# Kernel optimization log

Measured on AMD Instinct MI355X. Metric: run time of the kernel, lower is better.

Reference implementation:

```python
import jax, jax.numpy as jnp
import numpy as np

D_MODEL = 1024
NHEAD = 8
HEAD_DIM = D_MODEL // NHEAD
D_FF = 4096
EPS_ATTN = 1e-6
EPS_LN = 1e-5


def _layernorm(x, g, b):
    mu = jnp.mean(x, axis=-1, keepdims=True)
    var = jnp.var(x, axis=-1, keepdims=True)
    return (x - mu) * jax.lax.rsqrt(var + EPS_LN) * g + b


def _linear_attention(q, k, v):
    # q,k,v: [N, L, H, D]
    Q = jax.nn.elu(q) + 1.0
    K = jax.nn.elu(k) + 1.0
    v_length = v.shape[1]
    v = v / v_length
    KV = jnp.einsum('nshd,nshv->nhdv', K, v)           # [N,H,D,D]
    Z = 1.0 / (jnp.einsum('nlhd,nhd->nlh', Q, K.sum(axis=1)) + EPS_ATTN)
    out = jnp.einsum('nlhd,nhdv,nlh->nlhv', Q, KV, Z) * v_length
    return out


def setup_inputs() -> dict:
    key = jax.random.key(0)
    ks = jax.random.split(key, 12)
    s = 1.0 / np.sqrt(D_MODEL)
    sf = 1.0 / np.sqrt(D_FF)
    return {
        'x': jax.random.normal(ks[0], (2, 4096, D_MODEL), jnp.float32),
        'wq': jax.random.normal(ks[1], (D_MODEL, D_MODEL), jnp.float32) * s,
        'wk': jax.random.normal(ks[2], (D_MODEL, D_MODEL), jnp.float32) * s,
        'wv': jax.random.normal(ks[3], (D_MODEL, D_MODEL), jnp.float32) * s,
        'w1': jax.random.normal(ks[4], (D_FF, D_MODEL), jnp.float32) * s,
        'b1': jnp.zeros((D_FF,), jnp.float32),
        'w2': jax.random.normal(ks[5], (D_MODEL, D_FF), jnp.float32) * sf,
        'b2': jnp.zeros((D_MODEL,), jnp.float32),
        'g1': jnp.ones((D_MODEL,), jnp.float32),
        'be1': jnp.zeros((D_MODEL,), jnp.float32),
        'g2': jnp.ones((D_MODEL,), jnp.float32),
        'be2': jnp.zeros((D_MODEL,), jnp.float32),
    }


def reference(x, wq, wk, wv, w1, b1, w2, b2, g1, be1, g2, be2):
    N, L, C = x.shape
    # pre-norm self attention
    x2 = _layernorm(x, g1, be1)
    q = (x2 @ wq.T).reshape(N, L, NHEAD, HEAD_DIM)
    k = (x2 @ wk.T).reshape(N, L, NHEAD, HEAD_DIM)
    v = (x2 @ wv.T).reshape(N, L, NHEAD, HEAD_DIM)
    msg = _linear_attention(q, k, v).reshape(N, L, C)
    x = x + msg
    # MLP block
    x2 = _layernorm(x, g2, be2)
    h = jax.nn.gelu(x2 @ w1.T + b1, approximate=False)
    x = x + (h @ w2.T + b2)
    return x
```

## Files before the change

kernel.cpp:

```cpp
#include <hip/hip_runtime.h>
#include <hip/hip_bf16.h>
#include <math.h>

typedef __bf16 bf16x8 __attribute__((ext_vector_type(8)));
typedef float f32x4 __attribute__((ext_vector_type(4)));

#define DEVI __device__ __forceinline__

DEVI void gload_lds16(const __bf16* g, __bf16* l) {
    __builtin_amdgcn_global_load_lds(
        (const __attribute__((address_space(1))) void*)g,
        (__attribute__((address_space(3))) void*)l, 16, 0, 0);
}

__global__ void sniff_kernel(const unsigned short* __restrict__ x, int* flags) {
    const int tid = threadIdx.x;
    const unsigned short u = x[tid * 2];
    const int e = (u >> 7) & 0xFF;
    const int zero = (u == 0) ? 1 : 0;
    const int sane = ((e >= 0x71 && e <= 0x8E) || ((u & 0x7FFF) == 0)) ? 1 : 0;
    const unsigned long long mz = __ballot(zero != 0);
    const unsigned long long ms = __ballot(sane != 0);
    __shared__ int wz[4], wsn[4];
    if ((tid & 63) == 0) { wz[tid >> 6] = __popcll(mz); wsn[tid >> 6] = __popcll(ms); }
    __syncthreads();
    if (tid == 0) {
        const int nz = wz[0] + wz[1] + wz[2] + wz[3];
        const int ns = wsn[0] + wsn[1] + wsn[2] + wsn[3];
        flags[0] = (nz >= 192 || ns < 128) ? 1 : 0;
    }
}

__global__ __launch_bounds__(256) void convert_kernel(const void* __restrict__ src,
                                                      __bf16* __restrict__ dst, int n,
                                                      const int* __restrict__ flags) {
    const int i = (blockIdx.x * 256 + threadIdx.x) * 8;
    if (i >= n) return;
    if (flags[0]) {
        const float* s = (const float*)src;
        bf16x8 o;
#pragma unroll
        for (int j = 0; j < 8; j++) o[j] = (__bf16)s[i + j];
        *(bf16x8*)(dst + i) = o;
    } else {
        *(uint4*)(dst + i) = *(const uint4*)((const __bf16*)src + i);
    }
}

template <typename T>
__global__ __launch_bounds__(256) void ln_kernel(const T* __restrict__ x,
                                                 const __bf16* __restrict__ g,
                                                 const __bf16* __restrict__ b,
                                                 __bf16* __restrict__ out) {
    const size_t row = blockIdx.x;
    const T* xr = x + row * 1024;
    const int tid = threadIdx.x;
    float v[4];
#pragma unroll
    for (int i = 0; i < 4; i++) v[i] = (float)xr[tid * 4 + i];
    float s = v[0] + v[1] + v[2] + v[3];
    float s2 = v[0] * v[0] + v[1] * v[1] + v[2] * v[2] + v[3] * v[3];
#pragma unroll
    for (int m = 32; m >= 1; m >>= 1) {
        s += __shfl_xor(s, m, 64);
        s2 += __shfl_xor(s2, m, 64);
    }
    __shared__ float rs[4], rs2[4];
    const int wave = tid >> 6, lane = tid & 63;
    if (lane == 0) { rs[wave] = s; rs2[wave] = s2; }
    __syncthreads();
    s = rs[0] + rs[1] + rs[2] + rs[3];
    s2 = rs2[0] + rs2[1] + rs2[2] + rs2[3];
    const float mu = s * (1.0f / 1024.0f);
    const float var = s2 * (1.0f / 1024.0f) - mu * mu;
    const float inv = rsqrtf(var + 1e-5f);
#pragma unroll
    for (int i = 0; i < 4; i++) {
        const int c = tid * 4 + i;
        out[row * 1024 + c] = (__bf16)((v[i] - mu) * inv * (float)g[c] + (float)b[c]);
    }
}

enum { EP_NONE = 0, EP_ELU1 = 1, EP_BIAS_GELU = 2, EP_BIAS_RES = 3, EP_QKV = 4 };

#define READMM(RA, RB)                                                        \
    do {                                                                      \
        bf16x8 af_[4], bfv_[4];                                               \
        _Pragma("unroll") for (int i_ = 0; i_ < 4; i_++) {                    \
            af_[i_]  = *(const bf16x8*)&RA[(wm * 64 + i_ * 16 + lm) * 32 + swz]; \
            bfv_[i_] = *(const bf16x8*)&RB[(wn * 64 + i_ * 16 + lm) * 32 + swz]; \
        }                                                                     \
        _Pragma("unroll") for (int i_ = 0; i_ < 4; i_++)                      \
            _Pragma("unroll") for (int j_ = 0; j_ < 4; j_++)                  \
                acc[i_][j_] = __builtin_amdgcn_mfma_f32_16x16x32_bf16(        \
                    af_[i_], bfv_[j_], acc[i_][j_], 0, 0, 0);                 \
    } while (0)

#define KBODY(RA, RB, SA, SB, TS, WAITN)                                      \
    do {                                                                      \
        asm volatile("s_waitcnt vmcnt(" #WAITN ")" ::: "memory");             \
        __builtin_amdgcn_s_barrier();                                         \
        __builtin_amdgcn_sched_barrier(0);                                    \
        if ((TS) < nt) {                                                      \
            const int k0_ = (TS) << 5;                                        \
            gload_lds16(pa0 + k0_, &SA[tid * 8]);                             \
            gload_lds16(pa1 + k0_, &SA[2048 + tid * 8]);                      \
            gload_lds16(pb0 + k0_, &SB[tid * 8]);                             \
            gload_lds16(pb1 + k0_, &SB[2048 + tid * 8]);                      \
        }                                                                     \
        __builtin_amdgcn_s_setprio(1);                                        \
        READMM(RA, RB);                                                       \
        __builtin_amdgcn_s_setprio(0);                                        \
    } while (0)

template <int EP, typename OutT>
__global__ __launch_bounds__(256, 3) void gemm_bt(
    const __bf16* __restrict__ A, const __bf16* __restrict__ B,
    const __bf16* __restrict__ bias, const float* __restrict__ resid,
    OutT* __restrict__ C, int M, int N, int K) {
    const int gx = gridDim.x, gy = gridDim.y;
    int bm = blockIdx.y, bn = blockIdx.x;
    {
        const int nwg = gx * gy;
        if ((gx & 7) == 0 && (nwg & 63) == 0) {
            const int bid = bm * gx + bn;
            const int perx = nwg >> 3;
            const int gid = (bid & 7) * perx + (bid >> 3);
            const int stg = gid >> 6, pos = gid & 63;
            const int stw = gx >> 3;
            bm = (stg / stw) * 8 + (pos >> 3);
            bn = (stg % stw) * 8 + (pos & 7);
        }
    }
    const int tid = threadIdx.x;
    const int wave = tid >> 6, lane = tid & 63;
    const int wm = wave & 1, wn = wave >> 1;
    const int lm = lane & 15, lq = lane >> 4;
    const int swz = (lq ^ ((lm >> 1) & 3)) * 8;

    __shared__ __align__(16) __bf16 As0[128 * 32];
    __shared__ __align__(16) __bf16 As1[128 * 32];
    __shared__ __align__(16) __bf16 As2[128 * 32];
    __shared__ __align__(16) __bf16 Bs0[128 * 32];
    __shared__ __align__(16) __bf16 Bs1[128 * 32];
    __shared__ __align__(16) __bf16 Bs2[128 * 32];

    f32x4 acc[4][4] = {};

    const int sr = tid >> 2;
    const int sc = (((tid & 3) ^ ((tid >> 3) & 3)) << 3);

    const __bf16* pa0 = A + (size_t)(bm * 128 + sr) * K + sc;
    const __bf16* pa1 = pa0 + (size_t)64 * K;
    const __bf16* pb0 = B + (size_t)(bn * 128 + sr) * K + sc;
    const __bf16* pb1 = pb0 + (size_t)64 * K;

    const int nt = K >> 5;

    gload_lds16(pa0, &As0[tid * 8]);
    gload_lds16(pa1, &As0[2048 + tid * 8]);
    gload_lds16(pb0, &Bs0[tid * 8]);
    gload_lds16(pb1, &Bs0[2048 + tid * 8]);
    if (nt > 1) {
        gload_lds16(pa0 + 32, &As1[tid * 8]);
        gload_lds16(pa1 + 32, &As1[2048 + tid * 8]);
        gload_lds16(pb0 + 32, &Bs1[tid * 8]);
        gload_lds16(pb1 + 32, &Bs1[2048 + tid * 8]);
    }

    int t = 0;
    for (; t + 2 < nt; t += 3) {
        KBODY(As0, Bs0, As2, Bs2, t + 2, 4);
        KBODY(As1, Bs1, As0, Bs0, t + 3, 4);
        KBODY(As2, Bs2, As1, Bs1, t + 4, 4);
    }
    if (t < nt) {
        asm volatile("s_waitcnt vmcnt(0)" ::: "memory");
        __builtin_amdgcn_s_barrier();
        __builtin_amdgcn_sched_barrier(0);
        READMM(As0, Bs0);
        t++;
        if (t < nt) { READMM(As1, Bs1); }
    }

    const int row0 = bm * 128 + wm * 64;
    const int col0 = bn * 128 + wn * 64;
#pragma unroll
    for (int i = 0; i < 4; i++) {
#pragma unroll
        for (int j = 0; j < 4; j++) {
            const int col = col0 + j * 16 + lm;
#pragma unroll
            for (int r = 0; r < 4; r++) {
                const int row = row0 + i * 16 + lq * 4 + r;
                float v = acc[i][j][r];
                if (EP == EP_QKV) {
                    float vv = (col < 2048) ? ((v > 0.0f) ? (v + 1.0f) : expf(v)) : v;
                    __bf16* dst = (col < 1024) ? (__bf16*)C
                                : (col < 2048) ? (__bf16*)const_cast<__bf16*>(bias)
                                               : (__bf16*)const_cast<float*>(resid);
                    dst[(size_t)row * 1024 + (col & 1023)] = (__bf16)vv;
                } else {
                    if (EP == EP_ELU1) {
                        v = (v > 0.0f) ? (v + 1.0f) : expf(v);
                    } else if (EP == EP_BIAS_GELU) {
                        v += (float)bias[col];
                        v = 0.5f * v * (1.0f + erff(v * 0.70710678118654752f));
                    } else if (EP == EP_BIAS_RES) {
                        v += (float)bias[col];
                        v += resid[(size_t)row * N + col];
                    }
                    C[(size_t)row * N + col] = (OutT)v;
                }
            }
        }
    }
}

__global__ __launch_bounds__(256) void kv_kernel(const __bf16* __restrict__ Kf,
                                                 const __bf16* __restrict__ Vf,
                                                 float* __restrict__ pkv,
                                                 float* __restrict__ pks) {
    const int nh = blockIdx.x, sc = blockIdx.y;
    const int n = nh >> 3, h = nh & 7;
    const int tid = threadIdx.x;
    const int tv = tid & 15, td = tid >> 4;
    __shared__ __align__(16) __bf16 Kt[32 * 128];
    __shared__ __align__(16) __bf16 Vt[32 * 128];
    float acc[8][8] = {};
    float ks[8] = {};
    const size_t rowbase = (size_t)n * 4096 + (size_t)sc * 256;
    for (int s0 = 0; s0 < 256; s0 += 32) {
#pragma unroll
        for (int rep = 0; rep < 2; rep++) {
            const int s = tid + rep * 256;
            const int r = s >> 4, cs = (s & 15) * 8;
            const size_t gidx = (rowbase + s0 + r) * 1024 + h * 128 + cs;
            *(bf16x8*)&Kt[r * 128 + cs] = *(const bf16x8*)&Kf[gidx];
            *(bf16x8*)&Vt[r * 128 + cs] = *(const bf16x8*)&Vf[gidx];
        }
        __syncthreads();
#pragma unroll 4
        for (int s = 0; s < 32; s++) {
            const bf16x8 k8 = *(const bf16x8*)&Kt[s * 128 + td * 8];
            const bf16x8 v8 = *(const bf16x8*)&Vt[s * 128 + tv * 8];
            float kk[8], vv[8];
#pragma unroll
            for (int i = 0; i < 8; i++) { kk[i] = (float)k8[i]; vv[i] = (float)v8[i]; }
#pragma unroll
            for (int i = 0; i < 8; i++) {
                ks[i] += kk[i];
#pragma unroll
                for (int j = 0; j < 8; j++) acc[i][j] += kk[i] * vv[j];
            }
        }
        __syncthreads();
    }
    float* dst = pkv + ((size_t)sc * 16 + nh) * 16384;
#pragma unroll
    for (int i = 0; i < 8; i++)
#pragma unroll
        for (int j = 0; j < 8; j++)
            dst[(td * 8 + i) * 128 + tv * 8 + j] = acc[i][j];
    if (tv == 0) {
        float* ds2 = pks + ((size_t)sc * 16 + nh) * 128;
#pragma unroll
        for (int i = 0; i < 8; i++) ds2[td * 8 + i] = ks[i];
    }
}

__global__ __launch_bounds__(256) void kv_reduce(const float* __restrict__ pkv,
                                                 const float* __restrict__ pks,
                                                 __bf16* __restrict__ kvb,
                                                 float* __restrict__ ksf) {
    const int idx = blockIdx.x * 256 + threadIdx.x;
    float s = 0.0f;
#pragma unroll
    for (int c = 0; c < 16; c++) s += pkv[(size_t)c * 262144 + idx];
    kvb[idx] = (__bf16)s;
    if (idx < 2048) {
        float t = 0.0f;
#pragma unroll
        for (int c = 0; c < 16; c++) t += pks[c * 2048 + idx];
        ksf[idx] = t;
    }
}

__global__ __launch_bounds__(256) void z_kernel(const __bf16* __restrict__ Qf,
                                                const float* __restrict__ ksf,
                                                float* __restrict__ zbuf) {
    const int idx = blockIdx.x * 256 + threadIdx.x;
    const int h = idx & 7;
    const size_t row = (size_t)(idx >> 3);
    const __bf16* q = Qf + row * 1024 + h * 128;
    const float* ks = ksf + ((size_t)((row >> 12) * 8 + h)) * 128;
    float s = 0.0f;
    for (int d = 0; d < 128; d += 8) {
        const bf16x8 q8 = *(const bf16x8*)&q[d];
#pragma unroll
        for (int j = 0; j < 8; j++) s += (float)q8[j] * ks[d + j];
    }
    zbuf[idx] = 1.0f / (s + 1e-6f);
}

__global__ __launch_bounds__(256, 2) void attn_out_kernel(
    const __bf16* __restrict__ x, const __bf16* __restrict__ Qf,
    const __bf16* __restrict__ kvb, const float* __restrict__ zbuf,
    float* __restrict__ xmid) {
    const int nh = blockIdx.x, lc = blockIdx.y;
    const int n = nh >> 3, h = nh & 7;
    const int tid = threadIdx.x;
    __shared__ __align__(16) __bf16 KVs[128 * 128];
    __shared__ __align__(16) __bf16 Qs[64 * 128];
    __shared__ float Zs[64];
    const __bf16* kv = kvb + (size_t)nh * 16384;
    for (int i = tid * 8; i < 16384; i += 2048)
        *(bf16x8*)&KVs[i] = *(const bf16x8*)&kv[i];
    const size_t gr0 = (size_t)n * 4096 + (size_t)lc * 64;
#pragma unroll
    for (int rep = 0; rep < 4; rep++) {
        const int s = tid + rep * 256;
        const int r = s >> 4, cs = (s & 15) * 8;
        *(bf16x8*)&Qs[r * 128 + cs] = *(const bf16x8*)&Qf[(gr0 + r) * 1024 + h * 128 + cs];
    }
    if (tid < 64) Zs[tid] = zbuf[(gr0 + tid) * 8 + h];
    __syncthreads();
    const int tv = (tid & 15) * 8;
    const int tr0 = (tid >> 4) * 4;
    float acc[4][8] = {};
    for (int d = 0; d < 128; d++) {
        const bf16x8 kv8 = *(const bf16x8*)&KVs[d * 128 + tv];
        float kf[8];
#pragma unroll
        for (int j = 0; j < 8; j++) kf[j] = (float)kv8[j];
#pragma unroll
        for (int rr = 0; rr < 4; rr++) {
            const float q = (float)Qs[(tr0 + rr) * 128 + d];
#pragma unroll
            for (int j = 0; j < 8; j++) acc[rr][j] += q * kf[j];
        }
    }
#pragma unroll
    for (int rr = 0; rr < 4; rr++) {
        const size_t gi = (gr0 + tr0 + rr) * 1024 + h * 128 + tv;
        const float z = Zs[tr0 + rr];
        const bf16x8 xr = *(const bf16x8*)&x[gi];
#pragma unroll
        for (int j = 0; j < 8; j++) xmid[gi + j] = (float)xr[j] + acc[rr][j] * z;
    }
}

extern "C" void kernel_launch(void* const* d_in, const int* in_sizes, int n_in,
                              void* d_out, int out_size, void* d_ws, size_t ws_size,
                              hipStream_t stream) {
    float* out = (float*)d_out;
    char* ws = (char*)d_ws;

    const int nx = 8388608, nw = 1048576, nw1 = 4194304, nb1 = 4096, ng = 1024;
    size_t off = 0;
    __bf16* cx   = (__bf16*)(ws + off); off += (size_t)nx * 2;
    __bf16* cwq  = (__bf16*)(ws + off); off += (size_t)nw * 2;
    __bf16* cwk  = (__bf16*)(ws + off); off += (size_t)nw * 2;
    __bf16* cwv  = (__bf16*)(ws + off); off += (size_t)nw * 2;
    __bf16* cw1  = (__bf16*)(ws + off); off += (size_t)nw1 * 2;
    __bf16* cb1  = (__bf16*)(ws + off); off += (size_t)nb1 * 2;
    __bf16* cw2  = (__bf16*)(ws + off); off += (size_t)nw1 * 2;
    __bf16* cb2  = (__bf16*)(ws + off); off += (size_t)ng * 2;
    __bf16* cg1  = (__bf16*)(ws + off); off += (size_t)ng * 2;
    __bf16* cbe1 = (__bf16*)(ws + off); off += (size_t)ng * 2;
    __bf16* cg2  = (__bf16*)(ws + off); off += (size_t)ng * 2;
    __bf16* cbe2 = (__bf16*)(ws + off); off += (size_t)ng * 2;
    int* flags = (int*)(ws + off); off += 64;

    char* PB = ws + off;
    __bf16* x2   = (__bf16*)(PB);
    __bf16* Qf   = (__bf16*)(PB + 16777216);
    float*  pkv  = (float*)(PB + 33554432);
    __bf16* hbuf = (__bf16*)(PB + 16777216);
    __bf16* Kf   = (__bf16*)(PB + 50331648);
    __bf16* Vf   = (__bf16*)(PB + 67108864);
    float*  xmid = (float*)(PB + 50331648);
    float*  pks  = (float*)(PB + 83886080);
    float*  ksf  = (float*)(PB + 84017152);
    float*  zbuf = (float*)(PB + 84025344);
    __bf16* kvb  = (__bf16*)(PB + 84287488);

    sniff_kernel<<<1, 256, 0, stream>>>((const unsigned short*)d_in[0], flags);
    convert_kernel<<<nx / 2048, 256, 0, stream>>>(d_in[0], cx, nx, flags);
    convert_kernel<<<nw / 2048, 256, 0, stream>>>(d_in[1], cwq, nw, flags);
    convert_kernel<<<nw / 2048, 256, 0, stream>>>(d_in[2], cwk, nw, flags);
    convert_kernel<<<nw / 2048, 256, 0, stream>>>(d_in[3], cwv, nw, flags);
    convert_kernel<<<nw1 / 2048, 256, 0, stream>>>(d_in[4], cw1, nw1, flags);
    convert_kernel<<<2, 256, 0, stream>>>(d_in[5], cb1, nb1, flags);
    convert_kernel<<<nw1 / 2048, 256, 0, stream>>>(d_in[6], cw2, nw1, flags);
    convert_kernel<<<1, 256, 0, stream>>>(d_in[7], cb2, ng, flags);
    convert_kernel<<<1, 256, 0, stream>>>(d_in[8], cg1, ng, flags);
    convert_kernel<<<1, 256, 0, stream>>>(d_in[9], cbe1, ng, flags);
    convert_kernel<<<1, 256, 0, stream>>>(d_in[10], cg2, ng, flags);
    convert_kernel<<<1, 256, 0, stream>>>(d_in[11], cbe2, ng, flags);

    ln_kernel<__bf16><<<8192, 256, 0, stream>>>(cx, cg1, cbe1, x2);
    gemm_bt<EP_QKV, __bf16><<<dim3(3072 / 128, 8192 / 128), 256, 0, stream>>>(
        x2, cwq, (const __bf16*)Kf, (const float*)Vf, Qf, 8192, 3072, 1024);
    kv_kernel<<<dim3(16, 16), 256, 0, stream>>>(Kf, Vf, pkv, pks);
    kv_reduce<<<1024, 256, 0, stream>>>(pkv, pks, kvb, ksf);
    z_kernel<<<256, 256, 0, stream>>>(Qf, ksf, zbuf);
    attn_out_kernel<<<dim3(16, 64), 256, 0, stream>>>(cx, Qf, kvb, zbuf, xmid);
    ln_kernel<float><<<8192, 256, 0, stream>>>(xmid, cg2, cbe2, x2);
    for (int c = 0; c < 2; c++) {
        const size_t ro = (size_t)c * 4096;
        gemm_bt<EP_BIAS_GELU, __bf16><<<dim3(4096 / 128, 4096 / 128), 256, 0, stream>>>(
            x2 + ro * 1024, cw1, cb1, nullptr, hbuf, 4096, 4096, 1024);
        gemm_bt<EP_BIAS_RES, float><<<dim3(1024 / 128, 4096 / 128), 256, 0, stream>>>(
            hbuf, cw2, cb2, xmid + ro * 1024, out + ro * 1024, 4096, 1024, 4096);
    }
}
```

Measured before the change: 455.0 us.

## Add 256x256-tile 8-wave GEMM with split-K LDS pipeline for QKV and FC1

Adds a new GEMM kernel that uses 256x256 output tiles, 512 threads (8 waves, each computing a 128x64 sub-tile), and a double-buffered LDS pipeline that stages each 64-wide K step as two 32-wide halves. Finer-grained barriers interleave the global-to-LDS loads with the MFMA work. The QKV projection and the FC1+GELU GEMM now use this kernel, while FC2 stays on the old 128x128 kernel. The larger tiles are meant to raise arithmetic intensity and cut global/LDS traffic per FLOP. In exchange the kernel needs 128KB of LDS and many more accumulator registers, which lowers occupancy, and the fewer, larger workgroups may leave CUs idle at the tail.

```diff
diff --git a/kernel.cpp b/kernel.cpp
--- a/kernel.cpp
+++ b/kernel.cpp
@@ -83,34 +83,203 @@
 
 enum { EP_NONE = 0, EP_ELU1 = 1, EP_BIAS_GELU = 2, EP_BIAS_RES = 3, EP_QKV = 4 };
 
-#define READMM(RA, RB)                                                        \
-    do {                                                                      \
-        bf16x8 af_[4], bfv_[4];                                               \
-        _Pragma("unroll") for (int i_ = 0; i_ < 4; i_++) {                    \
-            af_[i_]  = *(const bf16x8*)&RA[(wm * 64 + i_ * 16 + lm) * 32 + swz]; \
+#define STG256(DST, P0, P1, KOFF)                         \
+    do {                                                  \
+        gload_lds16((P0) + (KOFF), &DST[tid * 8]);        \
+        gload_lds16((P1) + (KOFF), &DST[4096 + tid * 8]); \
+    } while (0)
+
+#define MFMA4x4(AV, BV, FRB)                                                   \
+    do {                                                                       \
+        _Pragma("unroll") for (int f_ = 0; f_ < 4; f_++)                       \
+            _Pragma("unroll") for (int c_ = 0; c_ < 4; c_++)                   \
+                acc[(FRB) + f_][c_] = __builtin_amdgcn_mfma_f32_16x16x32_bf16( \
+                    AV[f_], BV[c_], acc[(FRB) + f_][c_], 0, 0, 0);             \
+    } while (0)
+
+#define ITER256(RA0, RA1, RB0, RB1, SA0m, SA1m, SB0m, SB1m, TN, DO_STAGE, VM1) \
+    do {                                                                       \
+        bf16x8 a_[4];                                                          \
+                                    \
+        asm volatile("s_waitcnt vmcnt(4)" ::: "memory");                       \
+        __builtin_amdgcn_s_barrier();                                          \
+        __builtin_amdgcn_sched_barrier(0);                                     \
+        _Pragma("unroll") for (int f_ = 0; f_ < 4; f_++)                       \
+            b0[f_] = *(const bf16x8*)&RB0[boff[f_]];                           \
+        _Pragma("unroll") for (int f_ = 0; f_ < 4; f_++)                       \
+            a_[f_] = *(const bf16x8*)&RA0[aoff[f_]];                           \
+        if (DO_STAGE) STG256(SA0m, sA0, sA1, (TN) * 64);                       \
+        asm volatile("s_waitcnt lgkmcnt(0)" ::: "memory");                     \
+        __builtin_amdgcn_sched_barrier(0);                                     \
+        __builtin_amdgcn_s_setprio(1);                                         \
+        MFMA4x4(a_, b0, 0);                                                    \
+        __builtin_amdgcn_s_setprio(0);                                         \
+                                    \
+        asm volatile("s_waitcnt vmcnt(" #VM1 ")" ::: "memory");                \
+        __builtin_amdgcn_s_barrier();                                          \
+        __builtin_amdgcn_sched_barrier(0);                                     \
+        _Pragma("unroll") for (int f_ = 0; f_ < 4; f_++)                       \
+            b1[f_] = *(const bf16x8*)&RB1[boff[f_]];                           \
+        _Pragma("unroll") for (int f_ = 0; f_ < 4; f_++)                       \
+            a_[f_] = *(const bf16x8*)&RA1[aoff[f_]];                           \
+        if (DO_STAGE) STG256(SB0m, sB0, sB1, (TN) * 64);                       \
+        asm volatile("s_waitcnt lgkmcnt(0)" ::: "memory");                     \
+        __builtin_amdgcn_sched_barrier(0);                                     \
+        __builtin_amdgcn_s_setprio(1);                                         \
+        MFMA4x4(a_, b1, 0);                                                    \
+        __builtin_amdgcn_s_setprio(0);                                         \
+                              \
+        __builtin_amdgcn_s_barrier();                                          \
+        __builtin_amdgcn_sched_barrier(0);                                     \
+        _Pragma("unroll") for (int f_ = 0; f_ < 4; f_++)                       \
+            a_[f_] = *(const bf16x8*)&RA0[aoff[4 + f_]];                       \
+        if (DO_STAGE) STG256(SA1m, sA0, sA1, (TN) * 64 + 32);                  \
+        asm volatile("s_waitcnt lgkmcnt(0)" ::: "memory");                     \
+        __builtin_amdgcn_sched_barrier(0);                                     \
+        __builtin_amdgcn_s_setprio(1);                                         \
+        MFMA4x4(a_, b0, 4);                                                    \
+        __builtin_amdgcn_s_setprio(0);                                         \
+                              \
+        __builtin_amdgcn_s_barrier();                                          \
+        __builtin_amdgcn_sched_barrier(0);                                     \
+        _Pragma("unroll") for (int f_ = 0; f_ < 4; f_++)                       \
+            a_[f_] = *(const bf16x8*)&RA1[aoff[4 + f_]];                       \
+        if (DO_STAGE) STG256(SB1m, sB0, sB1, (TN) * 64 + 32);                  \
+        asm volatile("s_waitcnt lgkmcnt(0)" ::: "memory");                     \
+        __builtin_amdgcn_sched_barrier(0);                                     \
+        __builtin_amdgcn_s_setprio(1);                                         \
+        MFMA4x4(a_, b1, 4);                                                    \
+        __builtin_amdgcn_s_setprio(0);                                         \
+    } while (0)
+
+template <int EP>
+__global__ __launch_bounds__(512, 2) void gemm256(
+    const __bf16* __restrict__ A, const __bf16* __restrict__ B,
+    const __bf16* __restrict__ bias, __bf16* __restrict__ out2,
+    __bf16* __restrict__ out3, __bf16* __restrict__ C, int M, int N, int K) {
+    const int gx = gridDim.x, gy = gridDim.y;
+    int bm = blockIdx.y, bn = blockIdx.x;
+    {
+        const int nwg = gx * gy;
+        const int bid = bm * gx + bn;
+        if ((gx & 7) == 0 && (nwg & 63) == 0) {
+            const int perx = nwg >> 3;
+            const int gid = (bid & 7) * perx + (bid >> 3);
+            const int stg = gid >> 6, pos = gid & 63;
+            const int stw = gx >> 3;
+            bm = (stg / stw) * 8 + (pos >> 3);
+            bn = (stg % stw) * 8 + (pos & 7);
+        } else if ((nwg & 7) == 0) {
+            const int perx = nwg >> 3;
+            const int gid = (bid & 7) * perx + (bid >> 3);
+            bm = gid / gx;
+            bn = gid % gx;
+        }
+    }
+    const int tid = threadIdx.x;
+    const int wave = tid >> 6, lane = tid & 63;
+    const int wr = wave >> 2, wc = wave & 3;
+    const int lm = lane & 15, lq = lane >> 4;
+
+    __shared__ __align__(16) __bf16 A0k0[8192];
+    __shared__ __align__(16) __bf16 A0k1[8192];
+    __shared__ __align__(16) __bf16 B0k0[8192];
+    __shared__ __align__(16) __bf16 B0k1[8192];
+    __shared__ __align__(16) __bf16 A1k0[8192];
+    __shared__ __align__(16) __bf16 A1k1[8192];
+    __shared__ __align__(16) __bf16 B1k0[8192];
+    __shared__ __align__(16) __bf16 B1k1[8192];
+
+    f32x4 acc[8][4] = {};
+    bf16x8 b0[4], b1[4];
+
+    int aoff[8], boff[4];
+#pragma unroll
+    for (int fr = 0; fr < 8; fr++) {
+        const int row = wr * 128 + fr * 16 + lm;
+        aoff[fr] = row * 32 + ((lq ^ (lm & 3)) << 3);
+    }
+#pragma unroll
+    for (int fc = 0; fc < 4; fc++) {
+        const int row = wc * 64 + fc * 16 + lm;
+        boff[fc] = row * 32 + ((lq ^ (lm & 3)) << 3);
+    }
+
+    const int srow = tid >> 2;
+    const int sg = (((tid & 3) ^ ((tid >> 2) & 3)) << 3);
+    const __bf16* sA0 = A + (size_t)(bm * 256 + srow) * K + sg;
+    const __bf16* sA1 = sA0 + (size_t)128 * K;
+    const __bf16* sB0 = B + (size_t)(bn * 256 + srow) * K + sg;
+    const __bf16* sB1 = sB0 + (size_t)128 * K;
+
+    const int nt = K >> 6;
+
+    STG256(A0k0, sA0, sA1, 0);
+    STG256(B0k0, sB0, sB1, 0);
+    STG256(A0k1, sA0, sA1, 32);
+    STG256(B0k1, sB0, sB1, 32);
+
+    int t = 0;
+    for (; t + 2 < nt; t += 2) {
+        ITER256(A0k0, A0k1, B0k0, B0k1, A1k0, A1k1, B1k0, B1k1, t + 1, true, 2);
+        ITER256(A1k0, A1k1, B1k0, B1k1, A0k0, A0k1, B0k0, B0k1, t + 2, true, 2);
+    }
+    ITER256(A0k0, A0k1, B0k0, B0k1, A1k0, A1k1, B1k0, B1k1, t + 1, true, 2);
+    ITER256(A1k0, A1k1, B1k0, B1k1, A0k0, A0k1, B0k0, B0k1, 0, false, 0);
+
+    const int rowb = bm * 256 + wr * 128 + lq * 4;
+    const int colb = bn * 256 + wc * 64 + lm;
+#pragma unroll
+    for (int fr = 0; fr < 8; fr++) {
+#pragma unroll
+        for (int fc = 0; fc < 4; fc++) {
+            const int col = colb + fc * 16;
+#pragma unroll
+            for (int r = 0; r < 4; r++) {
+                const int row = rowb + fr * 16 + r;
+                float v = acc[fr][fc][r];
+                if (EP == EP_QKV) {
+                    float vv = (col < 2048) ? ((v > 0.0f) ? (v + 1.0f) : expf(v)) : v;
+                    __bf16* dst = (col < 1024) ? C : (col < 2048) ? out2 : out3;
+                    dst[(size_t)row * 1024 + (col & 1023)] = (__bf16)vv;
+                } else {
+                    v += (float)bias[col];
+                    v = 0.5f * v * (1.0f + erff(v * 0.70710678118654752f));
+                    C[(size_t)row * N + col] = (__bf16)v;
+                }
+            }
+        }
+    }
+}
+
+#define READMM(RA, RB)                                                           \
+    do {                                                                         \
+        bf16x8 af_[4], bfv_[4];                                                  \
+        _Pragma("unroll") for (int i_ = 0; i_ < 4; i_++) {                       \
+            af_[i_] = *(const bf16x8*)&RA[(wm * 64 + i_ * 16 + lm) * 32 + swz];  \
             bfv_[i_] = *(const bf16x8*)&RB[(wn * 64 + i_ * 16 + lm) * 32 + swz]; \
-        }                                                                     \
-        _Pragma("unroll") for (int i_ = 0; i_ < 4; i_++)                      \
-            _Pragma("unroll") for (int j_ = 0; j_ < 4; j_++)                  \
-                acc[i_][j_] = __builtin_amdgcn_mfma_f32_16x16x32_bf16(        \
-                    af_[i_], bfv_[j_], acc[i_][j_], 0, 0, 0);                 \
+        }                                                                        \
+        _Pragma("unroll") for (int i_ = 0; i_ < 4; i_++)                         \
+            _Pragma("unroll") for (int j_ = 0; j_ < 4; j_++)                     \
+                acc[i_][j_] = __builtin_amdgcn_mfma_f32_16x16x32_bf16(           \
+                    af_[i_], bfv_[j_], acc[i_][j_], 0, 0, 0);                    \
     } while (0)
 
-#define KBODY(RA, RB, SA, SB, TS, WAITN)                                      \
-    do {                                                                      \
-        asm volatile("s_waitcnt vmcnt(" #WAITN ")" ::: "memory");             \
-        __builtin_amdgcn_s_barrier();                                         \
-        __builtin_amdgcn_sched_barrier(0);                                    \
-        if ((TS) < nt) {                                                      \
-            const int k0_ = (TS) << 5;                                        \
-            gload_lds16(pa0 + k0_, &SA[tid * 8]);                             \
-            gload_lds16(pa1 + k0_, &SA[2048 + tid * 8]);                      \
-            gload_lds16(pb0 + k0_, &SB[tid * 8]);                             \
-            gload_lds16(pb1 + k0_, &SB[2048 + tid * 8]);                      \
-        }                                                                     \
-        __builtin_amdgcn_s_setprio(1);                                        \
-        READMM(RA, RB);                                                       \
-        __builtin_amdgcn_s_setprio(0);                                        \
+#define KBODY(RA, RB, SA, SB, TS, WAITN)                           \
+    do {                                                           \
+        asm volatile("s_waitcnt vmcnt(" #WAITN ")" ::: "memory");  \
+        __builtin_amdgcn_s_barrier();                              \
+        __builtin_amdgcn_sched_barrier(0);                         \
+        if ((TS) < nt) {                                           \
+            const int k0_ = (TS) << 5;                             \
+            gload_lds16(pa0 + k0_, &SA[tid * 8]);                  \
+            gload_lds16(pa1 + k0_, &SA[2048 + tid * 8]);           \
+            gload_lds16(pb0 + k0_, &SB[tid * 8]);                  \
+            gload_lds16(pb1 + k0_, &SB[2048 + tid * 8]);           \
+        }                                                          \
+        __builtin_amdgcn_s_setprio(1);                             \
+        READMM(RA, RB);                                            \
+        __builtin_amdgcn_s_setprio(0);                             \
     } while (0)
 
 template <int EP, typename OutT>
@@ -194,24 +363,16 @@
             for (int r = 0; r < 4; r++) {
                 const int row = row0 + i * 16 + lq * 4 + r;
                 float v = acc[i][j][r];
-                if (EP == EP_QKV) {
-                    float vv = (col < 2048) ? ((v > 0.0f) ? (v + 1.0f) : expf(v)) : v;
-                    __bf16* dst = (col < 1024) ? (__bf16*)C
-                                : (col < 2048) ? (__bf16*)const_cast<__bf16*>(bias)
-                                               : (__bf16*)const_cast<float*>(resid);
-                    dst[(size_t)row * 1024 + (col & 1023)] = (__bf16)vv;
-                } else {
-                    if (EP == EP_ELU1) {
-                        v = (v > 0.0f) ? (v + 1.0f) : expf(v);
-                    } else if (EP == EP_BIAS_GELU) {
-                        v += (float)bias[col];
-                        v = 0.5f * v * (1.0f + erff(v * 0.70710678118654752f));
-                    } else if (EP == EP_BIAS_RES) {
-                        v += (float)bias[col];
-                        v += resid[(size_t)row * N + col];
-                    }
-                    C[(size_t)row * N + col] = (OutT)v;
+                if (EP == EP_ELU1) {
+                    v = (v > 0.0f) ? (v + 1.0f) : expf(v);
+                } else if (EP == EP_BIAS_GELU) {
+                    v += (float)bias[col];
+                    v = 0.5f * v * (1.0f + erff(v * 0.70710678118654752f));
+                } else if (EP == EP_BIAS_RES) {
+                    v += (float)bias[col];
+                    v += resid[(size_t)row * N + col];
                 }
+                C[(size_t)row * N + col] = (OutT)v;
             }
         }
     }
@@ -400,8 +561,8 @@
     convert_kernel<<<1, 256, 0, stream>>>(d_in[11], cbe2, ng, flags);
 
     ln_kernel<__bf16><<<8192, 256, 0, stream>>>(cx, cg1, cbe1, x2);
-    gemm_bt<EP_QKV, __bf16><<<dim3(3072 / 128, 8192 / 128), 256, 0, stream>>>(
-        x2, cwq, (const __bf16*)Kf, (const float*)Vf, Qf, 8192, 3072, 1024);
+    gemm256<EP_QKV><<<dim3(3072 / 256, 8192 / 256), 512, 0, stream>>>(
+        x2, cwq, nullptr, Kf, Vf, Qf, 8192, 3072, 1024);
     kv_kernel<<<dim3(16, 16), 256, 0, stream>>>(Kf, Vf, pkv, pks);
     kv_reduce<<<1024, 256, 0, stream>>>(pkv, pks, kvb, ksf);
     z_kernel<<<256, 256, 0, stream>>>(Qf, ksf, zbuf);
@@ -409,8 +570,8 @@
     ln_kernel<float><<<8192, 256, 0, stream>>>(xmid, cg2, cbe2, x2);
     for (int c = 0; c < 2; c++) {
         const size_t ro = (size_t)c * 4096;
-        gemm_bt<EP_BIAS_GELU, __bf16><<<dim3(4096 / 128, 4096 / 128), 256, 0, stream>>>(
-            x2 + ro * 1024, cw1, cb1, nullptr, hbuf, 4096, 4096, 1024);
+        gemm256<EP_BIAS_GELU><<<dim3(4096 / 256, 4096 / 256), 512, 0, stream>>>(
+            x2 + ro * 1024, cw1, cb1, nullptr, nullptr, hbuf, 4096, 4096, 1024);
         gemm_bt<EP_BIAS_RES, float><<<dim3(1024 / 128, 4096 / 128), 256, 0, stream>>>(
             hbuf, cw2, cb2, xmid + ro * 1024, out + ro * 1024, 4096, 1024, 4096);
     }
```

New measurement: 465.0 us. 2.2% more time.

## Fuse Z normalizer into attention output and use 64-row tiles for down-projection

Applied to the files above, without the earlier changes.

The separate z_kernel is removed, and the Q·ksum dot product is now computed inside attn_out_kernel from a shared-memory copy of the key sums, avoiding a launch and a round trip through global memory. The gemm kernel gains a BM template parameter. The second MLP GEMM (N=1024, K=4096) uses 64-row tiles, which doubles its block count from 256 to 512 for better CU occupancy on a small grid. The cost is smaller per-block reuse of B tiles and extra FMAs per d-step in the attention loop.

```diff
diff --git a/kernel.cpp b/kernel.cpp
--- a/kernel.cpp
+++ b/kernel.cpp
@@ -83,37 +83,41 @@
 
 enum { EP_NONE = 0, EP_ELU1 = 1, EP_BIAS_GELU = 2, EP_BIAS_RES = 3, EP_QKV = 4 };
 
-#define READMM(RA, RB)                                                        \
-    do {                                                                      \
-        bf16x8 af_[4], bfv_[4];                                               \
-        _Pragma("unroll") for (int i_ = 0; i_ < 4; i_++) {                    \
-            af_[i_]  = *(const bf16x8*)&RA[(wm * 64 + i_ * 16 + lm) * 32 + swz]; \
-            bfv_[i_] = *(const bf16x8*)&RB[(wn * 64 + i_ * 16 + lm) * 32 + swz]; \
-        }                                                                     \
-        _Pragma("unroll") for (int i_ = 0; i_ < 4; i_++)                      \
-            _Pragma("unroll") for (int j_ = 0; j_ < 4; j_++)                  \
-                acc[i_][j_] = __builtin_amdgcn_mfma_f32_16x16x32_bf16(        \
-                    af_[i_], bfv_[j_], acc[i_][j_], 0, 0, 0);                 \
+#define READMM(RA, RB)                                                            \
+    do {                                                                          \
+        bf16x8 af_[BM / 32], bfv_[4];                                             \
+        _Pragma("unroll") for (int i_ = 0; i_ < BM / 32; i_++)                    \
+            af_[i_] = *(const bf16x8*)&RA[(wm * (BM / 2) + i_ * 16 + lm) * 32 + swz]; \
+        _Pragma("unroll") for (int j_ = 0; j_ < 4; j_++)                          \
+            bfv_[j_] = *(const bf16x8*)&RB[(wn * 64 + j_ * 16 + lm) * 32 + swz];  \
+        _Pragma("unroll") for (int i_ = 0; i_ < BM / 32; i_++)                    \
+            _Pragma("unroll") for (int j_ = 0; j_ < 4; j_++)                      \
+                acc[i_][j_] = __builtin_amdgcn_mfma_f32_16x16x32_bf16(            \
+                    af_[i_], bfv_[j_], acc[i_][j_], 0, 0, 0);                     \
     } while (0)
 
-#define KBODY(RA, RB, SA, SB, TS, WAITN)                                      \
-    do {                                                                      \
-        asm volatile("s_waitcnt vmcnt(" #WAITN ")" ::: "memory");             \
-        __builtin_amdgcn_s_barrier();                                         \
-        __builtin_amdgcn_sched_barrier(0);                                    \
-        if ((TS) < nt) {                                                      \
-            const int k0_ = (TS) << 5;                                        \
-            gload_lds16(pa0 + k0_, &SA[tid * 8]);                             \
-            gload_lds16(pa1 + k0_, &SA[2048 + tid * 8]);                      \
-            gload_lds16(pb0 + k0_, &SB[tid * 8]);                             \
-            gload_lds16(pb1 + k0_, &SB[2048 + tid * 8]);                      \
-        }                                                                     \
-        __builtin_amdgcn_s_setprio(1);                                        \
-        READMM(RA, RB);                                                       \
-        __builtin_amdgcn_s_setprio(0);                                        \
+#define KBODY(RA, RB, SA, SB, TS)                                  \
+    do {                                                           \
+        if constexpr (BM == 128)                                   \
+            asm volatile("s_waitcnt vmcnt(4)" ::: "memory");       \
+        else                                                       \
+            asm volatile("s_waitcnt vmcnt(3)" ::: "memory");       \
+        __builtin_amdgcn_s_barrier();                              \
+        __builtin_amdgcn_sched_barrier(0);                         \
+        if ((TS) < nt) {                                           \
+            const int k0_ = (TS) << 5;                             \
+            gload_lds16(pa0 + k0_, &SA[tid * 8]);                  \
+            if constexpr (BM == 128)                               \
+                gload_lds16(pa1 + k0_, &SA[2048 + tid * 8]);       \
+            gload_lds16(pb0 + k0_, &SB[tid * 8]);                  \
+            gload_lds16(pb1 + k0_, &SB[2048 + tid * 8]);           \
+        }                                                          \
+        __builtin_amdgcn_s_setprio(1);                             \
+        READMM(RA, RB);                                            \
+        __builtin_amdgcn_s_setprio(0);                             \
     } while (0)
 
-template <int EP, typename OutT>
+template <int EP, int BM, typename OutT>
 __global__ __launch_bounds__(256, 3) void gemm_bt(
     const __bf16* __restrict__ A, const __bf16* __restrict__ B,
     const __bf16* __restrict__ bias, const float* __restrict__ resid,
@@ -138,41 +142,41 @@
     const int lm = lane & 15, lq = lane >> 4;
     const int swz = (lq ^ ((lm >> 1) & 3)) * 8;
 
-    __shared__ __align__(16) __bf16 As0[128 * 32];
-    __shared__ __align__(16) __bf16 As1[128 * 32];
-    __shared__ __align__(16) __bf16 As2[128 * 32];
+    __shared__ __align__(16) __bf16 As0[BM * 32];
+    __shared__ __align__(16) __bf16 As1[BM * 32];
+    __shared__ __align__(16) __bf16 As2[BM * 32];
     __shared__ __align__(16) __bf16 Bs0[128 * 32];
     __shared__ __align__(16) __bf16 Bs1[128 * 32];
     __shared__ __align__(16) __bf16 Bs2[128 * 32];
 
-    f32x4 acc[4][4] = {};
+    f32x4 acc[BM / 32][4] = {};
 
     const int sr = tid >> 2;
     const int sc = (((tid & 3) ^ ((tid >> 3) & 3)) << 3);
 
-    const __bf16* pa0 = A + (size_t)(bm * 128 + sr) * K + sc;
-    const __bf16* pa1 = pa0 + (size_t)64 * K;
+    const __bf16* pa0 = A + (size_t)(bm * BM + sr) * K + sc;
+    const __bf16* pa1 = pa0 + (size_t)(BM == 128 ? 64 : 0) * K;
     const __bf16* pb0 = B + (size_t)(bn * 128 + sr) * K + sc;
     const __bf16* pb1 = pb0 + (size_t)64 * K;
 
     const int nt = K >> 5;
 
     gload_lds16(pa0, &As0[tid * 8]);
-    gload_lds16(pa1, &As0[2048 + tid * 8]);
+    if constexpr (BM == 128) gload_lds16(pa1, &As0[2048 + tid * 8]);
     gload_lds16(pb0, &Bs0[tid * 8]);
     gload_lds16(pb1, &Bs0[2048 + tid * 8]);
     if (nt > 1) {
         gload_lds16(pa0 + 32, &As1[tid * 8]);
-        gload_lds16(pa1 + 32, &As1[2048 + tid * 8]);
+        if constexpr (BM == 128) gload_lds16(pa1 + 32, &As1[2048 + tid * 8]);
         gload_lds16(pb0 + 32, &Bs1[tid * 8]);
         gload_lds16(pb1 + 32, &Bs1[2048 + tid * 8]);
     }
 
     int t = 0;
     for (; t + 2 < nt; t += 3) {
-        KBODY(As0, Bs0, As2, Bs2, t + 2, 4);
-        KBODY(As1, Bs1, As0, Bs0, t + 3, 4);
-        KBODY(As2, Bs2, As1, Bs1, t + 4, 4);
+        KBODY(As0, Bs0, As2, Bs2, t + 2);
+        KBODY(As1, Bs1, As0, Bs0, t + 3);
+        KBODY(As2, Bs2, As1, Bs1, t + 4);
     }
     if (t < nt) {
         asm volatile("s_waitcnt vmcnt(0)" ::: "memory");
@@ -183,10 +187,10 @@
         if (t < nt) { READMM(As1, Bs1); }
     }
 
-    const int row0 = bm * 128 + wm * 64;
+    const int row0 = bm * BM + wm * (BM / 2);
     const int col0 = bn * 128 + wn * 64;
 #pragma unroll
-    for (int i = 0; i < 4; i++) {
+    for (int i = 0; i < BM / 32; i++) {
 #pragma unroll
         for (int j = 0; j < 4; j++) {
             const int col = col0 + j * 16 + lm;
@@ -286,33 +290,16 @@
     }
 }
 
-__global__ __launch_bounds__(256) void z_kernel(const __bf16* __restrict__ Qf,
-                                                const float* __restrict__ ksf,
-                                                float* __restrict__ zbuf) {
-    const int idx = blockIdx.x * 256 + threadIdx.x;
-    const int h = idx & 7;
-    const size_t row = (size_t)(idx >> 3);
-    const __bf16* q = Qf + row * 1024 + h * 128;
-    const float* ks = ksf + ((size_t)((row >> 12) * 8 + h)) * 128;
-    float s = 0.0f;
-    for (int d = 0; d < 128; d += 8) {
-        const bf16x8 q8 = *(const bf16x8*)&q[d];
-#pragma unroll
-        for (int j = 0; j < 8; j++) s += (float)q8[j] * ks[d + j];
-    }
-    zbuf[idx] = 1.0f / (s + 1e-6f);
-}
-
 __global__ __launch_bounds__(256, 2) void attn_out_kernel(
     const __bf16* __restrict__ x, const __bf16* __restrict__ Qf,
-    const __bf16* __restrict__ kvb, const float* __restrict__ zbuf,
+    const __bf16* __restrict__ kvb, const float* __restrict__ ksf,
     float* __restrict__ xmid) {
     const int nh = blockIdx.x, lc = blockIdx.y;
     const int n = nh >> 3, h = nh & 7;
     const int tid = threadIdx.x;
     __shared__ __align__(16) __bf16 KVs[128 * 128];
     __shared__ __align__(16) __bf16 Qs[64 * 128];
-    __shared__ float Zs[64];
+    __shared__ float Ks[128];
     const __bf16* kv = kvb + (size_t)nh * 16384;
     for (int i = tid * 8; i < 16384; i += 2048)
         *(bf16x8*)&KVs[i] = *(const bf16x8*)&kv[i];
@@ -323,19 +310,22 @@
         const int r = s >> 4, cs = (s & 15) * 8;
         *(bf16x8*)&Qs[r * 128 + cs] = *(const bf16x8*)&Qf[(gr0 + r) * 1024 + h * 128 + cs];
     }
-    if (tid < 64) Zs[tid] = zbuf[(gr0 + tid) * 8 + h];
+    if (tid < 128) Ks[tid] = ksf[(size_t)nh * 128 + tid];
     __syncthreads();
     const int tv = (tid & 15) * 8;
     const int tr0 = (tid >> 4) * 4;
     float acc[4][8] = {};
+    float zs[4] = {};
     for (int d = 0; d < 128; d++) {
         const bf16x8 kv8 = *(const bf16x8*)&KVs[d * 128 + tv];
+        const float ksd = Ks[d];
         float kf[8];
 #pragma unroll
         for (int j = 0; j < 8; j++) kf[j] = (float)kv8[j];
 #pragma unroll
         for (int rr = 0; rr < 4; rr++) {
             const float q = (float)Qs[(tr0 + rr) * 128 + d];
+            zs[rr] += q * ksd;
 #pragma unroll
             for (int j = 0; j < 8; j++) acc[rr][j] += q * kf[j];
         }
@@ -343,7 +333,7 @@
 #pragma unroll
     for (int rr = 0; rr < 4; rr++) {
         const size_t gi = (gr0 + tr0 + rr) * 1024 + h * 128 + tv;
-        const float z = Zs[tr0 + rr];
+        const float z = 1.0f / (zs[rr] + 1e-6f);
         const bf16x8 xr = *(const bf16x8*)&x[gi];
 #pragma unroll
         for (int j = 0; j < 8; j++) xmid[gi + j] = (float)xr[j] + acc[rr][j] * z;
@@ -382,7 +372,6 @@
     float*  xmid = (float*)(PB + 50331648);
     float*  pks  = (float*)(PB + 83886080);
     float*  ksf  = (float*)(PB + 84017152);
-    float*  zbuf = (float*)(PB + 84025344);
     __bf16* kvb  = (__bf16*)(PB + 84287488);
 
     sniff_kernel<<<1, 256, 0, stream>>>((const unsigned short*)d_in[0], flags);
@@ -400,18 +389,17 @@
     convert_kernel<<<1, 256, 0, stream>>>(d_in[11], cbe2, ng, flags);
 
     ln_kernel<__bf16><<<8192, 256, 0, stream>>>(cx, cg1, cbe1, x2);
-    gemm_bt<EP_QKV, __bf16><<<dim3(3072 / 128, 8192 / 128), 256, 0, stream>>>(
+    gemm_bt<EP_QKV, 128, __bf16><<<dim3(3072 / 128, 8192 / 128), 256, 0, stream>>>(
         x2, cwq, (const __bf16*)Kf, (const float*)Vf, Qf, 8192, 3072, 1024);
     kv_kernel<<<dim3(16, 16), 256, 0, stream>>>(Kf, Vf, pkv, pks);
     kv_reduce<<<1024, 256, 0, stream>>>(pkv, pks, kvb, ksf);
-    z_kernel<<<256, 256, 0, stream>>>(Qf, ksf, zbuf);
-    attn_out_kernel<<<dim3(16, 64), 256, 0, stream>>>(cx, Qf, kvb, zbuf, xmid);
+    attn_out_kernel<<<dim3(16, 64), 256, 0, stream>>>(cx, Qf, kvb, ksf, xmid);
     ln_kernel<float><<<8192, 256, 0, stream>>>(xmid, cg2, cbe2, x2);
     for (int c = 0; c < 2; c++) {
         const size_t ro = (size_t)c * 4096;
-        gemm_bt<EP_BIAS_GELU, __bf16><<<dim3(4096 / 128, 4096 / 128), 256, 0, stream>>>(
+        gemm_bt<EP_BIAS_GELU, 128, __bf16><<<dim3(4096 / 128, 4096 / 128), 256, 0, stream>>>(
             x2 + ro * 1024, cw1, cb1, nullptr, hbuf, 4096, 4096, 1024);
-        gemm_bt<EP_BIAS_RES, float><<<dim3(1024 / 128, 4096 / 128), 256, 0, stream>>>(
+        gemm_bt<EP_BIAS_RES, 64, float><<<dim3(1024 / 128, 4096 / 64), 256, 0, stream>>>(
             hbuf, cw2, cb2, xmid + ro * 1024, out + ro * 1024, 4096, 1024, 4096);
     }
 }
```

Measured after the change: 441.7 us. -2.9%, faster.
